# Performance work log

Measured on AMD Instinct MI355X. Metric: run time of the kernel, lower is better.

The kernel has to match this reference:

```python
import jax, jax.numpy as jnp
import numpy as np
import math

D_MODEL = 512
NUM_HEADS = 8
D_K = D_MODEL // NUM_HEADS
MAX_LEN = 500
BATCH = 32
SEQ = 480


def setup_inputs() -> dict:
    key = jax.random.key(0)
    ks = jax.random.split(key, 10)
    s = 0.02
    x = jax.random.normal(ks[0], (BATCH, SEQ, D_MODEL), dtype=jnp.float32)
    wq = jax.random.normal(ks[1], (D_MODEL, D_MODEL), dtype=jnp.float32) * s
    bq = jnp.zeros((D_MODEL,), jnp.float32)
    wk = jax.random.normal(ks[2], (D_MODEL, D_MODEL), dtype=jnp.float32) * s
    bk = jnp.zeros((D_MODEL,), jnp.float32)
    wv = jax.random.normal(ks[3], (D_MODEL, D_MODEL), dtype=jnp.float32) * s
    bv = jnp.zeros((D_MODEL,), jnp.float32)
    wo = jax.random.normal(ks[4], (D_MODEL, D_MODEL), dtype=jnp.float32) * s
    bo = jnp.zeros((D_MODEL,), jnp.float32)
    rel_bias = jax.random.normal(ks[5], (NUM_HEADS, MAX_LEN, MAX_LEN), dtype=jnp.float32) * 0.02
    return {"x": x, "wq": wq, "bq": bq, "wk": wk, "bk": bk, "wv": wv,
            "bv": bv, "wo": wo, "bo": bo, "rel_bias": rel_bias}


def reference(x, wq, bq, wk, bk, wv, bv, wo, bo, rel_bias):
    B, S, D = x.shape
    H, dk = NUM_HEADS, D_K
    scale = math.sqrt(dk)
    # QKV projections -> [B, H, S, dk]
    q = (x @ wq + bq).reshape(B, S, H, dk).transpose(0, 2, 1, 3)
    k = (x @ wk + bk).reshape(B, S, H, dk).transpose(0, 2, 1, 3)
    v = (x @ wv + bv).reshape(B, S, H, dk).transpose(0, 2, 1, 3)
    scores = jnp.einsum('bhqd,bhkd->bhqk', q, k) / scale
    scores = scores + rel_bias[None, :, :S, :S]
    causal = jnp.triu(jnp.ones((S, S), dtype=bool), k=1)  # True where j > i
    scores = jnp.where(causal[None, None], -jnp.inf, scores)
    attn = jax.nn.softmax(scores, axis=-1)
    ctx = jnp.einsum('bhqk,bhkd->bhqd', attn, v)
    ctx = ctx.transpose(0, 2, 1, 3).reshape(B, S, D)
    out = ctx @ wo + bo
    return out, attn.mean(axis=1)
```

## Files before the change

kernel.cpp:

```cpp
#include <hip/hip_runtime.h>
#include <hip/hip_bf16.h>


typedef unsigned short ushort_t;
typedef __attribute__((ext_vector_type(8))) short short8;
typedef __attribute__((ext_vector_type(4))) float floatx4;

#define NB 32
#define NS 480
#define ND 512
#define NH 8
#define NDK 64
#define MAXLEN 500
#define KSTRIDE 72
#define BSTRIDE 68

__device__ __forceinline__ ushort_t f2bf(float f) {
  union { float f; unsigned u; } v; v.f = f;
  unsigned r = v.u + 0x7FFFu + ((v.u >> 16) & 1u);
  return (ushort_t)(r >> 16);
}

#define GLOAD_LDS16(g, l)                                                      \
  __builtin_amdgcn_global_load_lds(                                            \
      (const __attribute__((address_space(1))) void*)(g),                      \
      (__attribute__((address_space(3))) void*)(l), 16, 0, 0)

__global__ void cvt_x(const float* __restrict__ x, ushort_t* __restrict__ xb) {
  int idx = blockIdx.x * 256 + threadIdx.x;
  float4 v = ((const float4*)x)[idx];
  ushort4 o;
  o.x = f2bf(v.x); o.y = f2bf(v.y); o.z = f2bf(v.z); o.w = f2bf(v.w);
  ((ushort4*)xb)[idx] = o;
}

__global__ void cvt_w(const float* __restrict__ wq, const float* __restrict__ wk,
                      const float* __restrict__ wv, const float* __restrict__ wo,
                      ushort_t* __restrict__ wqT, ushort_t* __restrict__ wkT,
                      ushort_t* __restrict__ wvT, ushort_t* __restrict__ woT) {
  __shared__ float t[32][33];
  int z = blockIdx.z;
  const float* w = (z == 0) ? wq : (z == 1) ? wk : (z == 2) ? wv : wo;
  ushort_t* wT = (z == 0) ? wqT : (z == 1) ? wkT : (z == 2) ? wvT : woT;
  int k0 = blockIdx.x * 32, n0 = blockIdx.y * 32;
  int tx = threadIdx.x & 31, ty = threadIdx.x >> 5;
#pragma unroll
  for (int yy = 0; yy < 4; ++yy)
    t[ty + yy * 8][tx] = w[(k0 + ty + yy * 8) * ND + n0 + tx];
  __syncthreads();
#pragma unroll
  for (int yy = 0; yy < 4; ++yy)
    wT[(n0 + ty + yy * 8) * ND + k0 + tx] = f2bf(t[tx][ty + yy * 8]);
}

__global__ __launch_bounds__(256)
void qk_gemm(const ushort_t* __restrict__ xb,
             const ushort_t* __restrict__ wqT, const ushort_t* __restrict__ wkT,
             const float* __restrict__ bq, const float* __restrict__ bk,
             ushort_t* __restrict__ qb, ushort_t* __restrict__ kb) {
  __shared__ __align__(16) ushort_t sA[128 * 64];
  __shared__ __align__(16) ushort_t sB[128 * 64];
  const int tid = threadIdx.x;
  const int wid = tid >> 6, lane = tid & 63;
  const int lm = lane & 15, quad = lane >> 4;
  const int wr = wid >> 1, wc = wid & 1;
  const int row0 = blockIdx.x * 128;
  const int col0 = blockIdx.y * 128;
  const int z = blockIdx.z;
  const ushort_t* Bt = (z == 0) ? wqT : wkT;
  const float* bias = (z == 0) ? bq : bk;

  floatx4 zero4 = {0.f, 0.f, 0.f, 0.f};
  floatx4 acc[4][4];
#pragma unroll
  for (int i = 0; i < 4; ++i)
#pragma unroll
    for (int j = 0; j < 4; ++j) acc[i][j] = zero4;

  for (int k0 = 0; k0 < ND; k0 += 64) {
#pragma unroll
    for (int c = 0; c < 4; ++c) {
      int li = c * 256 + tid;
      int row = li >> 3, kc = li & 7;
      int kcs = kc ^ (row & 7);
      GLOAD_LDS16(xb + (row0 + row) * ND + k0 + kcs * 8, sA + (c * 256 + wid * 64) * 8);
      GLOAD_LDS16(Bt + (col0 + row) * ND + k0 + kcs * 8, sB + (c * 256 + wid * 64) * 8);
    }
    __syncthreads();
#pragma unroll
    for (int h2 = 0; h2 < 2; ++h2) {
      short8 a[4], b[4];
#pragma unroll
      for (int i = 0; i < 4; ++i) {
        int row = wr * 64 + i * 16 + lm;
        a[i] = *(const short8*)&sA[row * 64 + (((h2 << 2) | quad) ^ (lm & 7)) * 8];
      }
#pragma unroll
      for (int j = 0; j < 4; ++j) {
        int row = wc * 64 + j * 16 + lm;
        b[j] = *(const short8*)&sB[row * 64 + (((h2 << 2) | quad) ^ (lm & 7)) * 8];
      }
#pragma unroll
      for (int i = 0; i < 4; ++i)
#pragma unroll
        for (int j = 0; j < 4; ++j)
          acc[i][j] = __builtin_amdgcn_mfma_f32_16x16x32_bf16(a[i], b[j], acc[i][j], 0, 0, 0);
    }
    __syncthreads();
  }

  float bsv[4];
#pragma unroll
  for (int j = 0; j < 4; ++j) bsv[j] = bias[col0 + wc * 64 + j * 16 + lm];

#pragma unroll
  for (int i = 0; i < 4; ++i)
#pragma unroll
    for (int j = 0; j < 4; ++j)
#pragma unroll
      for (int r = 0; r < 4; ++r) {
        int m = row0 + wr * 64 + i * 16 + quad * 4 + r;
        int n = col0 + wc * 64 + j * 16 + lm;
        float val = acc[i][j][r] + bsv[j];
        int bb = m / NS, s = m - bb * NS;
        int h = n >> 6, d = n & 63;
        ushort_t o = f2bf(val);
        if (z == 0) qb[((bb * NH + h) * NS + s) * NDK + d] = o;
        else        kb[((bb * NH + h) * NS + s) * NDK + d] = o;
      }
}

__global__ __launch_bounds__(256)
void v_gemm(const ushort_t* __restrict__ xb, const ushort_t* __restrict__ wvT,
            const float* __restrict__ bv, ushort_t* __restrict__ vT) {
  __shared__ __align__(16) ushort_t sA[128 * 64];
  __shared__ __align__(16) ushort_t sB[128 * 64];
  const int tid = threadIdx.x;
  const int wid = tid >> 6, lane = tid & 63;
  const int lm = lane & 15, quad = lane >> 4;
  const int wr = wid >> 1, wc = wid & 1;
  const int row0 = blockIdx.x * 128;
  const int col0 = blockIdx.y * 128;
  const int b = blockIdx.z;
  const ushort_t* xbb = xb + (size_t)b * NS * ND;

  floatx4 zero4 = {0.f, 0.f, 0.f, 0.f};
  floatx4 acc[4][4];
#pragma unroll
  for (int i = 0; i < 4; ++i)
#pragma unroll
    for (int j = 0; j < 4; ++j) acc[i][j] = zero4;

  for (int k0 = 0; k0 < ND; k0 += 64) {
#pragma unroll
    for (int c = 0; c < 4; ++c) {
      int li = c * 256 + tid;
      int row = li >> 3, kc = li & 7;
      int kcs = kc ^ (row & 7);
      GLOAD_LDS16(wvT + (row0 + row) * ND + k0 + kcs * 8, sA + (c * 256 + wid * 64) * 8);
      int srow = min(col0 + row, NS - 1);
      GLOAD_LDS16(xbb + srow * ND + k0 + kcs * 8, sB + (c * 256 + wid * 64) * 8);
    }
    __syncthreads();
#pragma unroll
    for (int h2 = 0; h2 < 2; ++h2) {
      short8 a[4], b2[4];
#pragma unroll
      for (int i = 0; i < 4; ++i) {
        int row = wr * 64 + i * 16 + lm;
        a[i] = *(const short8*)&sA[row * 64 + (((h2 << 2) | quad) ^ (lm & 7)) * 8];
      }
#pragma unroll
      for (int j = 0; j < 4; ++j) {
        int row = wc * 64 + j * 16 + lm;
        b2[j] = *(const short8*)&sB[row * 64 + (((h2 << 2) | quad) ^ (lm & 7)) * 8];
      }
#pragma unroll
      for (int i = 0; i < 4; ++i)
#pragma unroll
        for (int j = 0; j < 4; ++j)
          acc[i][j] = __builtin_amdgcn_mfma_f32_16x16x32_bf16(a[i], b2[j], acc[i][j], 0, 0, 0);
    }
    __syncthreads();
  }

#pragma unroll
  for (int i = 0; i < 4; ++i)
#pragma unroll
    for (int r = 0; r < 4; ++r) {
      int m = row0 + wr * 64 + i * 16 + quad * 4 + r;
      float bias = bv[m];
#pragma unroll
      for (int j = 0; j < 4; ++j) {
        int n = col0 + wc * 64 + j * 16 + lm;
        if (n < NS)
          vT[((size_t)b * 512 + m) * NS + n] = f2bf(acc[i][j][r] + bias);
      }
    }
}

__global__ __launch_bounds__(256)
void flash_attn(const ushort_t* __restrict__ qb, const ushort_t* __restrict__ kb,
                const ushort_t* __restrict__ vT, const float* __restrict__ rel_bias,
                ushort_t* __restrict__ ctxb, float* __restrict__ cst) {
  const int bh = blockIdx.x;
  const int b = bh >> 3, h = bh & 7;
  const int qt = 7 - blockIdx.y;
  const int tid = threadIdx.x;
  const int wid = tid >> 6, lane = tid & 63;
  const int lm = lane & 15, quad = lane >> 4;

  __shared__ __align__(16) ushort_t sP[4][16 * 32];

  const int q0w = qt * 64 + wid * 16;
  if (q0w >= NS) return;

  const ushort_t* qh = qb + (size_t)bh * NS * NDK;
  const ushort_t* kh = kb + (size_t)bh * NS * NDK;
  const ushort_t* vh = vT + (size_t)bh * NDK * NS;

  short8 aq0 = *(const short8*)&qh[(q0w + lm) * NDK + quad * 8];
  short8 aq1 = *(const short8*)&qh[(q0w + lm) * NDK + 32 + quad * 8];

  float lsum[4];
  floatx4 O[4];
  floatx4 zero4 = {0.f, 0.f, 0.f, 0.f};
#pragma unroll
  for (int r = 0; r < 4; ++r) lsum[r] = 0.f;
#pragma unroll
  for (int jd = 0; jd < 4; ++jd) O[jd] = zero4;

  const int qmax = q0w + 15;
  const int nkt = qmax / 32 + 1;
  const int irow = q0w + quad * 4;

  for (int kt = 0; kt < nkt; ++kt) {
    const int kv0 = kt * 32 + 2 * lm;
    short8 bk00 = *(const short8*)&kh[kv0 * NDK + quad * 8];
    short8 bk01 = *(const short8*)&kh[kv0 * NDK + 32 + quad * 8];
    short8 bk10 = *(const short8*)&kh[(kv0 + 1) * NDK + quad * 8];
    short8 bk11 = *(const short8*)&kh[(kv0 + 1) * NDK + 32 + quad * 8];
    short8 bv2[4];
#pragma unroll
    for (int jd = 0; jd < 4; ++jd)
      bv2[jd] = *(const short8*)&vh[(jd * 16 + lm) * NS + kt * 32 + quad * 8];

    floatx4 s0 = zero4, s1 = zero4;
    s0 = __builtin_amdgcn_mfma_f32_16x16x32_bf16(aq0, bk00, s0, 0, 0, 0);
    s0 = __builtin_amdgcn_mfma_f32_16x16x32_bf16(aq1, bk01, s0, 0, 0, 0);
    s1 = __builtin_amdgcn_mfma_f32_16x16x32_bf16(aq0, bk10, s1, 0, 0, 0);
    s1 = __builtin_amdgcn_mfma_f32_16x16x32_bf16(aq1, bk11, s1, 0, 0, 0);

#pragma unroll
    for (int r = 0; r < 4; ++r) {
      int i = irow + r;
      float2 bb = *(const float2*)&rel_bias[((size_t)h * MAXLEN + i) * MAXLEN + kv0];
      float v0 = s0[r] * 0.125f + bb.x;
      float v1 = s1[r] * 0.125f + bb.y;
      if (kv0 > i) v0 = -1e30f;
      if (kv0 + 1 > i) v1 = -1e30f;
      float p0 = __expf(v0);
      float p1 = __expf(v1);
      lsum[r] += p0 + p1;
      unsigned packed = (unsigned)f2bf(p0) | ((unsigned)f2bf(p1) << 16);
      *(unsigned*)&sP[wid][(quad * 4 + r) * 32 + 2 * lm] = packed;
    }

    short8 ap = *(const short8*)&sP[wid][lm * 32 + quad * 8];
#pragma unroll
    for (int jd = 0; jd < 4; ++jd)
      O[jd] = __builtin_amdgcn_mfma_f32_16x16x32_bf16(ap, bv2[jd], O[jd], 0, 0, 0);
  }

#pragma unroll
  for (int off = 1; off < 16; off <<= 1)
#pragma unroll
    for (int r = 0; r < 4; ++r) lsum[r] += __shfl_xor(lsum[r], off, 64);

  float rinv[4];
#pragma unroll
  for (int r = 0; r < 4; ++r) rinv[r] = 1.f / lsum[r];
#pragma unroll
  for (int jd = 0; jd < 4; ++jd)
#pragma unroll
    for (int r = 0; r < 4; ++r)
      ctxb[((size_t)b * NS + irow + r) * ND + h * NDK + jd * 16 + lm] =
          f2bf(O[jd][r] * rinv[r]);
  if (lm == 0) {
#pragma unroll
    for (int r = 0; r < 4; ++r)
      cst[((size_t)b * NS + irow + r) * NH + h] = __logf(lsum[r]);
  }
}

__global__ __launch_bounds__(256)
void attn_mean_k(const ushort_t* __restrict__ qb, const ushort_t* __restrict__ kb,
                 const float* __restrict__ rel_bias, const float* __restrict__ cst,
                 float* __restrict__ attn_mean) {
  const int b = blockIdx.x;
  const int tile = blockIdx.y;
  const int it = tile >> 3, jt = tile & 7;
  const int tid = threadIdx.x;

  if (jt > it) {
    int r = tid >> 2;
    int i = it * 64 + r;
    if (i < NS) {
      float4 z = {0.f, 0.f, 0.f, 0.f};
#pragma unroll
      for (int cc = 0; cc < 4; ++cc) {
        int j = jt * 64 + (tid & 3) * 16 + cc * 4;
        if (j < NS) *(float4*)&attn_mean[((size_t)b * NS + i) * NS + j] = z;
      }
    }
    return;
  }

  __shared__ __align__(16) ushort_t sK[2][64 * KSTRIDE];
  __shared__ __align__(16) float sB[2][64 * BSTRIDE];

  const int wid = tid >> 6, lane = tid & 63;
  const int lm = lane & 15, quad = lane >> 4;
  const int i0 = it * 64 + wid * 16;
  const bool active = (i0 < NS);
  const int j0t = jt * 64;

  float cstv[4][8];
#pragma unroll
  for (int r = 0; r < 4; ++r) {
    int i = min(i0 + quad * 4 + r, NS - 1);
    float4 c0 = *(const float4*)&cst[((size_t)b * NS + i) * NH];
    float4 c1 = *(const float4*)&cst[((size_t)b * NS + i) * NH + 4];
    cstv[r][0] = c0.x; cstv[r][1] = c0.y; cstv[r][2] = c0.z; cstv[r][3] = c0.w;
    cstv[r][4] = c1.x; cstv[r][5] = c1.y; cstv[r][6] = c1.z; cstv[r][7] = c1.w;
  }

  const int krow0 = tid >> 3, koff = (tid & 7) * 8;
  const int brow0 = tid >> 4, boff = (tid & 15) * 4;
  const int kr0 = min(j0t + krow0, NS - 1);
  const int kr1 = min(j0t + krow0 + 32, NS - 1);

  uint4 kreg[2];
  float4 breg[4];
  short8 qa0, qa1, qn0, qn1;

  {
    const ushort_t* kh = kb + (size_t)(b * NH) * NS * NDK;
    kreg[0] = *(const uint4*)&kh[kr0 * NDK + koff];
    kreg[1] = *(const uint4*)&kh[kr1 * NDK + koff];
#pragma unroll
    for (int c = 0; c < 4; ++c) {
      int ri = min(it * 64 + brow0 + c * 16, NS - 1);
      breg[c] = *(const float4*)&rel_bias[((size_t)0 * MAXLEN + ri) * MAXLEN + j0t + boff];
    }
    const ushort_t* qh = qb + (size_t)(b * NH) * NS * NDK;
    int qi = min(i0 + lm, NS - 1);
    qa0 = *(const short8*)&qh[qi * NDK + quad * 8];
    qa1 = *(const short8*)&qh[qi * NDK + 32 + quad * 8];
    *(uint4*)&sK[0][krow0 * KSTRIDE + koff] = kreg[0];
    *(uint4*)&sK[0][(krow0 + 32) * KSTRIDE + koff] = kreg[1];
#pragma unroll
    for (int c = 0; c < 4; ++c)
      *(float4*)&sB[0][(brow0 + c * 16) * BSTRIDE + boff] = breg[c];
  }
  __syncthreads();

  floatx4 zero4 = {0.f, 0.f, 0.f, 0.f};
  floatx4 acc[4];
#pragma unroll
  for (int jj = 0; jj < 4; ++jj) acc[jj] = zero4;

#pragma unroll
  for (int h = 0; h < NH; ++h) {
    const int buf = h & 1;
    if (h < NH - 1) {
      const ushort_t* kh = kb + (size_t)(b * NH + h + 1) * NS * NDK;
      kreg[0] = *(const uint4*)&kh[kr0 * NDK + koff];
      kreg[1] = *(const uint4*)&kh[kr1 * NDK + koff];
#pragma unroll
      for (int c = 0; c < 4; ++c) {
        int ri = min(it * 64 + brow0 + c * 16, NS - 1);
        breg[c] = *(const float4*)&rel_bias[((size_t)(h + 1) * MAXLEN + ri) * MAXLEN +
                                            j0t + boff];
      }
      const ushort_t* qh = qb + (size_t)(b * NH + h + 1) * NS * NDK;
      int qi = min(i0 + lm, NS - 1);
      qn0 = *(const short8*)&qh[qi * NDK + quad * 8];
      qn1 = *(const short8*)&qh[qi * NDK + 32 + quad * 8];
    }

#pragma unroll
    for (int jj = 0; jj < 4; ++jj) {
      short8 bk0 = *(const short8*)&sK[buf][(jj * 16 + lm) * KSTRIDE + quad * 8];
      short8 bk1 = *(const short8*)&sK[buf][(jj * 16 + lm) * KSTRIDE + 32 + quad * 8];
      floatx4 s = zero4;
      s = __builtin_amdgcn_mfma_f32_16x16x32_bf16(qa0, bk0, s, 0, 0, 0);
      s = __builtin_amdgcn_mfma_f32_16x16x32_bf16(qa1, bk1, s, 0, 0, 0);
#pragma unroll
      for (int r = 0; r < 4; ++r) {
        float bias = sB[buf][(quad * 4 + r) * BSTRIDE + jj * 16 + lm];
        float p = __expf(s[r] * 0.125f + bias - cstv[r][h]);
        int i = i0 + quad * 4 + r;
        int j = j0t + jj * 16 + lm;
        if (j > i) p = 0.f;
        acc[jj][r] += p;
      }
    }

    if (h < NH - 1) {
      *(uint4*)&sK[buf ^ 1][krow0 * KSTRIDE + koff] = kreg[0];
      *(uint4*)&sK[buf ^ 1][(krow0 + 32) * KSTRIDE + koff] = kreg[1];
#pragma unroll
      for (int c = 0; c < 4; ++c)
        *(float4*)&sB[buf ^ 1][(brow0 + c * 16) * BSTRIDE + boff] = breg[c];
      qa0 = qn0; qa1 = qn1;
    }
    __syncthreads();
  }

  if (active) {
#pragma unroll
    for (int jj = 0; jj < 4; ++jj) {
      int j = j0t + jj * 16 + lm;
      if (j < NS) {
#pragma unroll
        for (int r = 0; r < 4; ++r)
          attn_mean[((size_t)b * NS + i0 + quad * 4 + r) * NS + j] =
              acc[jj][r] * 0.125f;
      }
    }
  }
}

__global__ __launch_bounds__(256)
void out_gemm(const ushort_t* __restrict__ ctxb, const ushort_t* __restrict__ woT,
              const float* __restrict__ bo, float* __restrict__ out) {
  __shared__ __align__(16) ushort_t sA[128 * 64];
  __shared__ __align__(16) ushort_t sB[128 * 64];
  const int tid = threadIdx.x;
  const int wid = tid >> 6, lane = tid & 63;
  const int lm = lane & 15, quad = lane >> 4;
  const int wr = wid >> 1, wc = wid & 1;
  const int row0 = blockIdx.x * 128;
  const int col0 = blockIdx.y * 128;

  floatx4 zero4 = {0.f, 0.f, 0.f, 0.f};
  floatx4 acc[4][4];
#pragma unroll
  for (int i = 0; i < 4; ++i)
#pragma unroll
    for (int j = 0; j < 4; ++j) acc[i][j] = zero4;

  for (int k0 = 0; k0 < ND; k0 += 64) {
#pragma unroll
    for (int c = 0; c < 4; ++c) {
      int li = c * 256 + tid;
      int row = li >> 3, kc = li & 7;
      int kcs = kc ^ (row & 7);
      GLOAD_LDS16(ctxb + (row0 + row) * ND + k0 + kcs * 8, sA + (c * 256 + wid * 64) * 8);
      GLOAD_LDS16(woT + (col0 + row) * ND + k0 + kcs * 8, sB + (c * 256 + wid * 64) * 8);
    }
    __syncthreads();
#pragma unroll
    for (int h2 = 0; h2 < 2; ++h2) {
      short8 a[4], b[4];
#pragma unroll
      for (int i = 0; i < 4; ++i) {
        int row = wr * 64 + i * 16 + lm;
        a[i] = *(const short8*)&sA[row * 64 + (((h2 << 2) | quad) ^ (lm & 7)) * 8];
      }
#pragma unroll
      for (int j = 0; j < 4; ++j) {
        int row = wc * 64 + j * 16 + lm;
        b[j] = *(const short8*)&sB[row * 64 + (((h2 << 2) | quad) ^ (lm & 7)) * 8];
      }
#pragma unroll
      for (int i = 0; i < 4; ++i)
#pragma unroll
        for (int j = 0; j < 4; ++j)
          acc[i][j] = __builtin_amdgcn_mfma_f32_16x16x32_bf16(a[i], b[j], acc[i][j], 0, 0, 0);
    }
    __syncthreads();
  }

  float bsv[4];
#pragma unroll
  for (int j = 0; j < 4; ++j) bsv[j] = bo[col0 + wc * 64 + j * 16 + lm];

#pragma unroll
  for (int i = 0; i < 4; ++i)
#pragma unroll
    for (int j = 0; j < 4; ++j)
#pragma unroll
      for (int r = 0; r < 4; ++r) {
        int m = row0 + wr * 64 + i * 16 + quad * 4 + r;
        int n = col0 + wc * 64 + j * 16 + lm;
        out[m * ND + n] = acc[i][j][r] + bsv[j];
      }
}

extern "C" void kernel_launch(void* const* d_in, const int* in_sizes, int n_in,
                              void* d_out, int out_size, void* d_ws, size_t ws_size,
                              hipStream_t stream) {
  const float* x  = (const float*)d_in[0];
  const float* wq = (const float*)d_in[1];
  const float* bq = (const float*)d_in[2];
  const float* wk = (const float*)d_in[3];
  const float* bk = (const float*)d_in[4];
  const float* wv = (const float*)d_in[5];
  const float* bv = (const float*)d_in[6];
  const float* wo = (const float*)d_in[7];
  const float* bo = (const float*)d_in[8];
  const float* rel_bias = (const float*)d_in[9];

  char* w = (char*)d_ws;
  ushort_t* xb  = (ushort_t*)w;
  ushort_t* wqT = (ushort_t*)(w + 15728640);
  ushort_t* wkT = wqT + 262144;
  ushort_t* wvT = wkT + 262144;
  ushort_t* woT = wvT + 262144;
  ushort_t* qb  = (ushort_t*)(w + 15728640 + 4 * 524288);
  ushort_t* kb  = qb + 7864320;
  ushort_t* vTb = kb + 7864320;
  ushort_t* ctxb = vTb + 7864320;
  float* cstat = (float*)(w + 15728640 + 4 * 524288 + 4 * 15728640);

  float* out0 = (float*)d_out;
  float* attn_mean = out0 + 7864320;

  cvt_x<<<dim3(7680), dim3(256), 0, stream>>>(x, xb);
  cvt_w<<<dim3(16, 16, 4), dim3(256), 0, stream>>>(wq, wk, wv, wo, wqT, wkT, wvT, woT);
  qk_gemm<<<dim3(120, 4, 2), dim3(256), 0, stream>>>(xb, wqT, wkT, bq, bk, qb, kb);
  v_gemm<<<dim3(4, 4, 32), dim3(256), 0, stream>>>(xb, wvT, bv, vTb);
  flash_attn<<<dim3(256, 8), dim3(256), 0, stream>>>(qb, kb, vTb, rel_bias, ctxb,
                                                     cstat);
  attn_mean_k<<<dim3(32, 64), dim3(256), 0, stream>>>(qb, kb, rel_bias, cstat,
                                                      attn_mean);
  out_gemm<<<dim3(120, 4), dim3(256), 0, stream>>>(ctxb, woT, bo, out0);
}
```

Before: 261.8 us.

## Process 32 query rows per wave in flash_attn with tiled V and bias

Each wave in flash_attn now handles two 16-row query groups, so every K and V fragment it loads feeds twice as many MFMAs. The causal tile count per wave is derived from the wave index, and the grid shrinks accordingly. V is written by v_gemm in a 64x32 tiled layout. A new cvt_rbt kernel re-lays rel_bias into per-key-tile contiguous blocks, stored in the no-longer-needed xb workspace, and the P scratch in LDS is padded. The aim is less global load traffic per unit of compute and more contiguous accesses. The cost is an extra kernel launch that rewrites the bias each call, plus more registers per wave, which may lower occupancy.

```diff
diff --git a/kernel.cpp b/kernel.cpp
--- a/kernel.cpp
+++ b/kernel.cpp
@@ -14,6 +14,7 @@
 #define MAXLEN 500
 #define KSTRIDE 72
 #define BSTRIDE 68
+#define PSTR 36
 
 __device__ __forceinline__ ushort_t f2bf(float f) {
   union { float f; unsigned u; } v; v.f = f;
@@ -51,6 +52,16 @@
 #pragma unroll
   for (int yy = 0; yy < 4; ++yy)
     wT[(n0 + ty + yy * 8) * ND + k0 + tx] = f2bf(t[tx][ty + yy * 8]);
+}
+
+__global__ void cvt_rbt(const float* __restrict__ rel_bias, float* __restrict__ rbt) {
+  int kt = blockIdx.x, ib = blockIdx.y, h = blockIdx.z;
+  int lm = threadIdx.x & 15, ii = threadIdx.x >> 4;
+  int i = ib * 16 + ii;
+  float f0 = rel_bias[((size_t)h * MAXLEN + i) * MAXLEN + kt * 32 + lm];
+  float f1 = rel_bias[((size_t)h * MAXLEN + i) * MAXLEN + kt * 32 + 16 + lm];
+  float2 o = {f0, f1};
+  *(float2*)&rbt[(((size_t)h * 15 + kt) * NS + i) * 32 + 2 * lm] = o;
 }
 
 __global__ __launch_bounds__(256)
@@ -132,7 +143,7 @@
 
 __global__ __launch_bounds__(256)
 void v_gemm(const ushort_t* __restrict__ xb, const ushort_t* __restrict__ wvT,
-            const float* __restrict__ bv, ushort_t* __restrict__ vT) {
+            const float* __restrict__ bv, ushort_t* __restrict__ vtil) {
   __shared__ __align__(16) ushort_t sA[128 * 64];
   __shared__ __align__(16) ushort_t sB[128 * 64];
   const int tid = threadIdx.x;
@@ -193,103 +204,132 @@
 #pragma unroll
       for (int j = 0; j < 4; ++j) {
         int n = col0 + wc * 64 + j * 16 + lm;
-        if (n < NS)
-          vT[((size_t)b * 512 + m) * NS + n] = f2bf(acc[i][j][r] + bias);
+        if (n < NS) {
+          size_t idx = (((size_t)b * NH + (m >> 6)) * 15 + (n >> 5)) * 2048 +
+                       (m & 63) * 32 + (n & 31);
+          vtil[idx] = f2bf(acc[i][j][r] + bias);
+        }
       }
     }
 }
 
 __global__ __launch_bounds__(256)
 void flash_attn(const ushort_t* __restrict__ qb, const ushort_t* __restrict__ kb,
-                const ushort_t* __restrict__ vT, const float* __restrict__ rel_bias,
+                const ushort_t* __restrict__ vtil, const float* __restrict__ rbt,
                 ushort_t* __restrict__ ctxb, float* __restrict__ cst) {
   const int bh = blockIdx.x;
   const int b = bh >> 3, h = bh & 7;
-  const int qt = 7 - blockIdx.y;
   const int tid = threadIdx.x;
   const int wid = tid >> 6, lane = tid & 63;
   const int lm = lane & 15, quad = lane >> 4;
 
-  __shared__ __align__(16) ushort_t sP[4][16 * 32];
-
-  const int q0w = qt * 64 + wid * 16;
-  if (q0w >= NS) return;
+  __shared__ __align__(16) ushort_t sP[4][32 * PSTR];
+
+  const int t = 14 - (blockIdx.y * 4 + wid);
+  if (t < 0) return;
+  const int nkt = t + 1;
 
   const ushort_t* qh = qb + (size_t)bh * NS * NDK;
   const ushort_t* kh = kb + (size_t)bh * NS * NDK;
-  const ushort_t* vh = vT + (size_t)bh * NDK * NS;
-
-  short8 aq0 = *(const short8*)&qh[(q0w + lm) * NDK + quad * 8];
-  short8 aq1 = *(const short8*)&qh[(q0w + lm) * NDK + 32 + quad * 8];
-
-  float lsum[4];
-  floatx4 O[4];
+  const ushort_t* vb = vtil + (size_t)bh * 15 * 2048;
+  const float* rb = rbt + (size_t)h * 15 * NS * 32;
+
+  short8 aq[2][2];
+#pragma unroll
+  for (int g = 0; g < 2; ++g) {
+    aq[g][0] = *(const short8*)&qh[(t * 32 + g * 16 + lm) * NDK + quad * 8];
+    aq[g][1] = *(const short8*)&qh[(t * 32 + g * 16 + lm) * NDK + 32 + quad * 8];
+  }
+
+  float lsum[2][4];
+  floatx4 O[2][4];
   floatx4 zero4 = {0.f, 0.f, 0.f, 0.f};
 #pragma unroll
-  for (int r = 0; r < 4; ++r) lsum[r] = 0.f;
-#pragma unroll
-  for (int jd = 0; jd < 4; ++jd) O[jd] = zero4;
-
-  const int qmax = q0w + 15;
-  const int nkt = qmax / 32 + 1;
-  const int irow = q0w + quad * 4;
+  for (int g = 0; g < 2; ++g) {
+#pragma unroll
+    for (int r = 0; r < 4; ++r) lsum[g][r] = 0.f;
+#pragma unroll
+    for (int jd = 0; jd < 4; ++jd) O[g][jd] = zero4;
+  }
 
   for (int kt = 0; kt < nkt; ++kt) {
-    const int kv0 = kt * 32 + 2 * lm;
-    short8 bk00 = *(const short8*)&kh[kv0 * NDK + quad * 8];
-    short8 bk01 = *(const short8*)&kh[kv0 * NDK + 32 + quad * 8];
-    short8 bk10 = *(const short8*)&kh[(kv0 + 1) * NDK + quad * 8];
-    short8 bk11 = *(const short8*)&kh[(kv0 + 1) * NDK + 32 + quad * 8];
+    const int kvA = kt * 32 + lm;
+    const int kvB = kvA + 16;
+    short8 bkA0 = *(const short8*)&kh[kvA * NDK + quad * 8];
+    short8 bkA1 = *(const short8*)&kh[kvA * NDK + 32 + quad * 8];
+    short8 bkB0 = *(const short8*)&kh[kvB * NDK + quad * 8];
+    short8 bkB1 = *(const short8*)&kh[kvB * NDK + 32 + quad * 8];
     short8 bv2[4];
 #pragma unroll
     for (int jd = 0; jd < 4; ++jd)
-      bv2[jd] = *(const short8*)&vh[(jd * 16 + lm) * NS + kt * 32 + quad * 8];
-
-    floatx4 s0 = zero4, s1 = zero4;
-    s0 = __builtin_amdgcn_mfma_f32_16x16x32_bf16(aq0, bk00, s0, 0, 0, 0);
-    s0 = __builtin_amdgcn_mfma_f32_16x16x32_bf16(aq1, bk01, s0, 0, 0, 0);
-    s1 = __builtin_amdgcn_mfma_f32_16x16x32_bf16(aq0, bk10, s1, 0, 0, 0);
-    s1 = __builtin_amdgcn_mfma_f32_16x16x32_bf16(aq1, bk11, s1, 0, 0, 0);
-
-#pragma unroll
-    for (int r = 0; r < 4; ++r) {
-      int i = irow + r;
-      float2 bb = *(const float2*)&rel_bias[((size_t)h * MAXLEN + i) * MAXLEN + kv0];
-      float v0 = s0[r] * 0.125f + bb.x;
-      float v1 = s1[r] * 0.125f + bb.y;
-      if (kv0 > i) v0 = -1e30f;
-      if (kv0 + 1 > i) v1 = -1e30f;
-      float p0 = __expf(v0);
-      float p1 = __expf(v1);
-      lsum[r] += p0 + p1;
-      unsigned packed = (unsigned)f2bf(p0) | ((unsigned)f2bf(p1) << 16);
-      *(unsigned*)&sP[wid][(quad * 4 + r) * 32 + 2 * lm] = packed;
-    }
-
-    short8 ap = *(const short8*)&sP[wid][lm * 32 + quad * 8];
+      bv2[jd] = *(const short8*)&vb[kt * 2048 + (jd * 16 + lm) * 32 + quad * 8];
+
+    floatx4 sA[2], sB[2];
+#pragma unroll
+    for (int g = 0; g < 2; ++g) {
+      floatx4 s = zero4;
+      s = __builtin_amdgcn_mfma_f32_16x16x32_bf16(aq[g][0], bkA0, s, 0, 0, 0);
+      s = __builtin_amdgcn_mfma_f32_16x16x32_bf16(aq[g][1], bkA1, s, 0, 0, 0);
+      sA[g] = s;
+      s = zero4;
+      s = __builtin_amdgcn_mfma_f32_16x16x32_bf16(aq[g][0], bkB0, s, 0, 0, 0);
+      s = __builtin_amdgcn_mfma_f32_16x16x32_bf16(aq[g][1], bkB1, s, 0, 0, 0);
+      sB[g] = s;
+    }
+
+#pragma unroll
+    for (int g = 0; g < 2; ++g)
+#pragma unroll
+      for (int r = 0; r < 4; ++r) {
+        int i = t * 32 + g * 16 + quad * 4 + r;
+        float2 bb = *(const float2*)&rb[((size_t)kt * NS + i) * 32 + 2 * lm];
+        float v0 = sA[g][r] * 0.125f + bb.x;
+        float v1 = sB[g][r] * 0.125f + bb.y;
+        if (kvA > i) v0 = -1e30f;
+        if (kvB > i) v1 = -1e30f;
+        float p0 = __expf(v0);
+        float p1 = __expf(v1);
+        lsum[g][r] += p0 + p1;
+        sP[wid][(g * 16 + quad * 4 + r) * PSTR + lm] = f2bf(p0);
+        sP[wid][(g * 16 + quad * 4 + r) * PSTR + 16 + lm] = f2bf(p1);
+      }
+
+#pragma unroll
+    for (int g = 0; g < 2; ++g) {
+      short8 ap = *(const short8*)&sP[wid][(g * 16 + lm) * PSTR + quad * 8];
+#pragma unroll
+      for (int jd = 0; jd < 4; ++jd)
+        O[g][jd] = __builtin_amdgcn_mfma_f32_16x16x32_bf16(ap, bv2[jd], O[g][jd], 0, 0, 0);
+    }
+  }
+
+#pragma unroll
+  for (int off = 1; off < 16; off <<= 1)
+#pragma unroll
+    for (int g = 0; g < 2; ++g)
+#pragma unroll
+      for (int r = 0; r < 4; ++r) lsum[g][r] += __shfl_xor(lsum[g][r], off, 64);
+
+#pragma unroll
+  for (int g = 0; g < 2; ++g) {
+    float rinv[4];
+#pragma unroll
+    for (int r = 0; r < 4; ++r) rinv[r] = 1.f / lsum[g][r];
 #pragma unroll
     for (int jd = 0; jd < 4; ++jd)
-      O[jd] = __builtin_amdgcn_mfma_f32_16x16x32_bf16(ap, bv2[jd], O[jd], 0, 0, 0);
-  }
-
-#pragma unroll
-  for (int off = 1; off < 16; off <<= 1)
-#pragma unroll
-    for (int r = 0; r < 4; ++r) lsum[r] += __shfl_xor(lsum[r], off, 64);
-
-  float rinv[4];
-#pragma unroll
-  for (int r = 0; r < 4; ++r) rinv[r] = 1.f / lsum[r];
-#pragma unroll
-  for (int jd = 0; jd < 4; ++jd)
-#pragma unroll
-    for (int r = 0; r < 4; ++r)
-      ctxb[((size_t)b * NS + irow + r) * ND + h * NDK + jd * 16 + lm] =
-          f2bf(O[jd][r] * rinv[r]);
-  if (lm == 0) {
-#pragma unroll
-    for (int r = 0; r < 4; ++r)
-      cst[((size_t)b * NS + irow + r) * NH + h] = __logf(lsum[r]);
+#pragma unroll
+      for (int r = 0; r < 4; ++r) {
+        int i = t * 32 + g * 16 + quad * 4 + r;
+        ctxb[((size_t)b * NS + i) * ND + h * NDK + jd * 16 + lm] =
+            f2bf(O[g][jd][r] * rinv[r]);
+      }
+    if (lm == 0) {
+#pragma unroll
+      for (int r = 0; r < 4; ++r) {
+        int i = t * 32 + g * 16 + quad * 4 + r;
+        cst[((size_t)b * NS + i) * NH + h] = __logf(lsum[g][r]);
+      }
+    }
   }
 }
 
@@ -521,9 +561,10 @@
   ushort_t* woT = wvT + 262144;
   ushort_t* qb  = (ushort_t*)(w + 15728640 + 4 * 524288);
   ushort_t* kb  = qb + 7864320;
-  ushort_t* vTb = kb + 7864320;
-  ushort_t* ctxb = vTb + 7864320;
+  ushort_t* vtil = kb + 7864320;
+  ushort_t* ctxb = vtil + 7864320;
   float* cstat = (float*)(w + 15728640 + 4 * 524288 + 4 * 15728640);
+  float* rbt = (float*)w;
 
   float* out0 = (float*)d_out;
   float* attn_mean = out0 + 7864320;
@@ -531,9 +572,9 @@
   cvt_x<<<dim3(7680), dim3(256), 0, stream>>>(x, xb);
   cvt_w<<<dim3(16, 16, 4), dim3(256), 0, stream>>>(wq, wk, wv, wo, wqT, wkT, wvT, woT);
   qk_gemm<<<dim3(120, 4, 2), dim3(256), 0, stream>>>(xb, wqT, wkT, bq, bk, qb, kb);
-  v_gemm<<<dim3(4, 4, 32), dim3(256), 0, stream>>>(xb, wvT, bv, vTb);
-  flash_attn<<<dim3(256, 8), dim3(256), 0, stream>>>(qb, kb, vTb, rel_bias, ctxb,
-                                                     cstat);
+  v_gemm<<<dim3(4, 4, 32), dim3(256), 0, stream>>>(xb, wvT, bv, vtil);
+  cvt_rbt<<<dim3(15, 30, 8), dim3(256), 0, stream>>>(rel_bias, rbt);
+  flash_attn<<<dim3(256, 4), dim3(256), 0, stream>>>(qb, kb, vtil, rbt, ctxb, cstat);
   attn_mean_k<<<dim3(32, 64), dim3(256), 0, stream>>>(qb, kb, rel_bias, cstat,
                                                       attn_mean);
   out_gemm<<<dim3(120, 4), dim3(256), 0, stream>>>(ctxb, woT, bo, out0);
```

New measurement: 250.0 us. 4.5% less time.
